# Kernel optimization log

Measured on AMD Instinct MI355X. Metric: run time of the kernel, lower is better.

Reference implementation:

```python
import jax, jax.numpy as jnp
import numpy as np

D_MODEL = 2048
K_SIZE = 4
GROUPS = 2048  # depthwise


def setup_inputs() -> dict:
    key = jax.random.key(0)
    k1, k2, k3, k4 = jax.random.split(key, 4)
    B, S, D = 4, 4096, D_MODEL
    x = jax.random.normal(k1, (B, S, D), dtype=jnp.float32)
    # nn.Linear(d_model, 3*d_model, bias=False): weight [3D, D], y = x @ W.T
    w1 = jax.random.normal(k2, (3 * D, D), dtype=jnp.float32) * (1.0 / np.sqrt(D))
    w2 = jax.random.normal(k3, (D, D), dtype=jnp.float32) * (1.0 / np.sqrt(D))
    # nn.Conv1d depthwise weight: [out_ch=D, in_ch/groups=1, k]
    conv_w = jax.random.normal(k4, (D, 1, K_SIZE), dtype=jnp.float32) * (1.0 / np.sqrt(K_SIZE))
    return {"x": x, "w1": w1, "w2": w2, "conv_w": conv_w}


def reference(x, w1, w2, conv_w):
    # x: [B, S, D]
    BCx = jnp.einsum("bsd,ed->bse", x, w1)  # [B, S, 3D]
    Bg, Cg, Xg = jnp.split(BCx, 3, axis=-1)  # each [B, S, D]
    gated = Bg * Xg
    # depthwise causal conv: torch pads k-1 both sides then slices [:seq_len]
    # == left-pad only k-1 (causal)
    y = jax.lax.conv_general_dilated(
        gated.transpose(0, 2, 1),          # [B, D, S]
        conv_w,                            # [D, 1, K]
        window_strides=(1,),
        padding=[(K_SIZE - 1, 0)],
        feature_group_count=GROUPS,
        dimension_numbers=("NCH", "OIH", "NCH"),
    )                                       # [B, D, S]
    conv_out = y.transpose(0, 2, 1)         # [B, S, D]
    out = jnp.einsum("bsd,ed->bse", Cg * conv_out, w2)  # [B, S, D]
    return out
```

## Files before the change

kernel.cpp:

```cpp
#include <hip/hip_runtime.h>
#include <stdint.h>

typedef unsigned short u16;
typedef __bf16 bf16x8 __attribute__((ext_vector_type(8)));
typedef float  f32x4  __attribute__((ext_vector_type(4)));

#define D_MODEL 2048
#define SEQ     4096
#define NROWS   16384
#define THREE_D 6144
#define K_SIZE  4
#define KC      2048
#define NT      64

__device__ __forceinline__ float b2f(u16 u) {
    union { uint32_t i; float f; } v; v.i = ((uint32_t)u) << 16; return v.f;
}
__device__ __forceinline__ u16 f2b(float f) {
    uint32_t u = __builtin_bit_cast(uint32_t, f);
    u += 0x7fff + ((u >> 16) & 1);
    return (u16)(u >> 16);
}

__global__ __launch_bounds__(256) void cast_f32_to_bf16(
    const float* __restrict__ src, u16* __restrict__ dst, int n8)
{
    int i = blockIdx.x * blockDim.x + threadIdx.x;
    if (i >= n8) return;
    const float4* s = (const float4*)src + (size_t)i * 2;
    float4 a = s[0], b = s[1];
    union { u16 u[8]; uint4 v; } o;
    o.u[0] = f2b(a.x); o.u[1] = f2b(a.y); o.u[2] = f2b(a.z); o.u[3] = f2b(a.w);
    o.u[4] = f2b(b.x); o.u[5] = f2b(b.y); o.u[6] = f2b(b.z); o.u[7] = f2b(b.w);
    *(uint4*)(dst + (size_t)i * 8) = o.v;
}

__global__ __launch_bounds__(256) void prep_cwt(
    const float* __restrict__ cw, float* __restrict__ cwt)
{
    int i = blockIdx.x * blockDim.x + threadIdx.x;
    if (i >= D_MODEL * K_SIZE) return;
    int d = i >> 2, k = i & 3;
    cwt[k * D_MODEL + d] = cw[i];
}

#define GLDS(gp, lp) __builtin_amdgcn_global_load_lds( \
    (const __attribute__((address_space(1))) void*)(gp), \
    (__attribute__((address_space(3))) void*)(lp), 16, 0, 0)

template<int BF16OUT>
__global__ __launch_bounds__(512, 2) void gemm256(
    const u16* __restrict__ A, const u16* __restrict__ B,
    void* __restrict__ Cout, int N, int n_per_xcd)
{
    __shared__ __align__(16) u16 lds[65536];

    const int tid  = threadIdx.x;
    const int lane = tid & 63;
    const int wave = tid >> 6;

    const int idx   = blockIdx.x;
    const int xcd   = idx & 7;
    const int local = idx >> 3;
    const int bm  = local / n_per_xcd;
    const int bn  = xcd * n_per_xcd + (local - bm * n_per_xcd);

    const int sfr  = tid & 15;
    const int sfq  = (tid >> 4) & 3;
    const int srow = (tid >> 6) * 16 + sfr;
    const size_t sK = (size_t)KC;
    const u16* ga = A + ((size_t)(bm * 256) + srow) * sK + sfq * 8;
    const u16* gb = B + ((size_t)(bn * 256) + srow) * sK + sfq * 8;

    u16* dst0 = lds + wave * 512;

    const int fr = lane & 15;
    const int fq = lane >> 4;
    const int wm = (wave >> 2) * 128;
    const int wn = (wave & 3) * 64;
    const int aBase = (wave >> 2) * 4096 + fq * 128 + fr * 8;
    const int bBase = 8192 + (wave & 3) * 2048 + fq * 128 + fr * 8;

    f32x4 acc[8][4] = {};

    #pragma unroll
    for (int t = 0; t < 3; t++) {
        u16* d = dst0 + t * 16384;
        const int kk = t * 32;
        GLDS(ga + kk,            d);
        GLDS(ga + 128 * sK + kk, d + 4096);
        GLDS(gb + kk,            d + 8192);
        GLDS(gb + 128 * sK + kk, d + 12288);
        __builtin_amdgcn_sched_barrier(0);
    }
    asm volatile("s_waitcnt vmcnt(8)" ::: "memory");
    __builtin_amdgcn_s_barrier();
    __builtin_amdgcn_sched_barrier(0);

    for (int t = 0; t < NT; t++) {
        const int buf = t & 3;
        if (t + 3 < NT) {
            u16* d = dst0 + ((t + 3) & 3) * 16384;
            const int kk = (t + 3) * 32;
            GLDS(ga + kk,            d);
            GLDS(ga + 128 * sK + kk, d + 4096);
            GLDS(gb + kk,            d + 8192);
            GLDS(gb + 128 * sK + kk, d + 12288);
        }
        __builtin_amdgcn_sched_barrier(0);

        bf16x8 a[8], b[4];
        const u16* la = lds + buf * 16384 + aBase;
        const u16* lb = lds + buf * 16384 + bBase;
        #pragma unroll
        for (int i = 0; i < 8; i++) a[i] = *(const bf16x8*)(la + i * 512);
        #pragma unroll
        for (int j = 0; j < 4; j++) b[j] = *(const bf16x8*)(lb + j * 512);

        __builtin_amdgcn_s_setprio(1);
        #pragma unroll
        for (int i = 0; i < 8; i++)
            #pragma unroll
            for (int j = 0; j < 4; j++)
                acc[i][j] = __builtin_amdgcn_mfma_f32_16x16x32_bf16(
                    a[i], b[j], acc[i][j], 0, 0, 0);
        __builtin_amdgcn_s_setprio(0);

        asm volatile("s_waitcnt lgkmcnt(0)" ::: "memory");
        __builtin_amdgcn_sched_barrier(0);
        if (t < NT - 3) {
            asm volatile("s_waitcnt vmcnt(8)" ::: "memory");
        } else if (t == NT - 3) {
            asm volatile("s_waitcnt vmcnt(4)" ::: "memory");
        } else if (t == NT - 2) {
            asm volatile("s_waitcnt vmcnt(0)" ::: "memory");
        }
        __builtin_amdgcn_s_barrier();
        __builtin_amdgcn_sched_barrier(0);
    }

    const int row0 = bm * 256 + wm + fq * 4;
    const int col0 = bn * 256 + wn + fr;
    if (BF16OUT) {
        u16* C = (u16*)Cout;
        #pragma unroll
        for (int i = 0; i < 8; i++)
            #pragma unroll
            for (int j = 0; j < 4; j++)
                #pragma unroll
                for (int r = 0; r < 4; r++)
                    C[(size_t)(row0 + i * 16 + r) * N + (col0 + j * 16)] = f2b(acc[i][j][r]);
    } else {
        float* C = (float*)Cout;
        #pragma unroll
        for (int i = 0; i < 8; i++)
            #pragma unroll
            for (int j = 0; j < 4; j++)
                #pragma unroll
                for (int r = 0; r < 4; r++)
                    C[(size_t)(row0 + i * 16 + r) * N + (col0 + j * 16)] = acc[i][j][r];
    }
}

__global__ __launch_bounds__(256) void gate_conv(
    const u16* __restrict__ BCx, const float* __restrict__ cwt, u16* __restrict__ z)
{
    const int n  = blockIdx.x;
    const int dg = threadIdx.x << 3;
    const int s  = n & (SEQ - 1);
    const u16* base = BCx + (size_t)n * THREE_D;

    float conv[8];
    #pragma unroll
    for (int j = 0; j < 8; j++) conv[j] = 0.f;

    #pragma unroll
    for (int r = 0; r < 4; r++) {
        const int back = 3 - r;
        if (s >= back) {
            const u16* pb = base - (size_t)back * THREE_D + dg;
            union { uint4 v; u16 u[8]; } ub, ux;
            ub.v = *(const uint4*)pb;
            ux.v = *(const uint4*)(pb + 2 * D_MODEL);
            const float* w = cwt + r * D_MODEL + dg;
            float4 w0 = *(const float4*)w;
            float4 w1 = *(const float4*)(w + 4);
            float ww[8] = { w0.x, w0.y, w0.z, w0.w, w1.x, w1.y, w1.z, w1.w };
            #pragma unroll
            for (int j = 0; j < 8; j++)
                conv[j] += b2f(ub.u[j]) * b2f(ux.u[j]) * ww[j];
        }
    }

    union { uint4 v; u16 u[8]; } uc, uo;
    uc.v = *(const uint4*)(base + D_MODEL + dg);
    #pragma unroll
    for (int j = 0; j < 8; j++)
        uo.u[j] = f2b(b2f(uc.u[j]) * conv[j]);
    *(uint4*)(z + (size_t)n * D_MODEL + dg) = uo.v;
}

extern "C" void kernel_launch(void* const* d_in, const int* in_sizes, int n_in,
                              void* d_out, int out_size, void* d_ws, size_t ws_size,
                              hipStream_t stream) {
    const float* x  = (const float*)d_in[0];
    const float* w1 = (const float*)d_in[1];
    const float* w2 = (const float*)d_in[2];
    const float* cw = (const float*)d_in[3];
    float* out = (float*)d_out;

    char* ws = (char*)d_ws;
    u16*   xb  = (u16*)(ws);
    u16*   w1b = (u16*)(ws + 67108864);
    u16*   w2b = (u16*)(ws + 92274688);
    float* cwt = (float*)(ws + 100663296);
    u16*   bcx = (u16*)(ws + 100696064);
    u16*   z   = (u16*)(ws + 302022656);

    cast_f32_to_bf16<<<dim3((4194304 + 255) / 256), 256, 0, stream>>>(x,  xb,  4194304);
    cast_f32_to_bf16<<<dim3((1572864 + 255) / 256), 256, 0, stream>>>(w1, w1b, 1572864);
    cast_f32_to_bf16<<<dim3((524288  + 255) / 256), 256, 0, stream>>>(w2, w2b, 524288);
    prep_cwt<<<dim3(32), 256, 0, stream>>>(cw, cwt);

    gemm256<1><<<dim3(1536), 512, 0, stream>>>(xb, w1b, (void*)bcx, THREE_D, 3);
    gate_conv<<<dim3(NROWS), 256, 0, stream>>>(bcx, cwt, z);
    gemm256<0><<<dim3(512), 512, 0, stream>>>(z, w2b, (void*)out, D_MODEL, 1);
}
```

Baseline: 933.3 us.

## Restructure GEMM mainloop into 64-wide K tiles with quadrant-interleaved staging

```diff
diff --git a/kernel.cpp b/kernel.cpp
--- a/kernel.cpp
+++ b/kernel.cpp
@@ -11,7 +11,7 @@
 #define THREE_D 6144
 #define K_SIZE  4
 #define KC      2048
-#define NT      64
+#define NK      32
 
 __device__ __forceinline__ float b2f(u16 u) {
     union { uint32_t i; float f; } v; v.i = ((uint32_t)u) << 16; return v.f;
@@ -57,7 +57,7 @@
 
     const int tid  = threadIdx.x;
     const int lane = tid & 63;
-    const int wave = tid >> 6;
+    const int wv   = tid >> 6;
 
     const int idx   = blockIdx.x;
     const int xcd   = idx & 7;
@@ -65,80 +65,96 @@
     const int bm  = local / n_per_xcd;
     const int bn  = xcd * n_per_xcd + (local - bm * n_per_xcd);
 
-    const int sfr  = tid & 15;
-    const int sfq  = (tid >> 4) & 3;
-    const int srow = (tid >> 6) * 16 + sfr;
+    const int sfr = tid & 15;
+    const int sfq = (tid >> 4) & 3;
+    const int gA0 = (wv & 3) + (wv >> 2) * 8;
+    const int gB0 = (wv & 1) + ((wv >> 1) & 3) * 4;
     const size_t sK = (size_t)KC;
-    const u16* ga = A + ((size_t)(bm * 256) + srow) * sK + sfq * 8;
-    const u16* gb = B + ((size_t)(bn * 256) + srow) * sK + sfq * 8;
-
-    u16* dst0 = lds + wave * 512;
+    const u16* Ab = A + ((size_t)(bm * 256) + sfr) * sK + sfq * 8;
+    const u16* Bb = B + ((size_t)(bn * 256) + sfr) * sK + sfq * 8;
+
+#define STAGE_A(g, b, k64) { \
+    GLDS(Ab + (size_t)((g) * 16) * sK + (k64),      lds + (b) * 32768 +         (g) * 512 + lane * 8); \
+    GLDS(Ab + (size_t)((g) * 16) * sK + (k64) + 32, lds + (b) * 32768 +  8192 + (g) * 512 + lane * 8); }
+#define STAGE_B(g, b, k64) { \
+    GLDS(Bb + (size_t)((g) * 16) * sK + (k64),      lds + (b) * 32768 + 16384 + (g) * 512 + lane * 8); \
+    GLDS(Bb + (size_t)((g) * 16) * sK + (k64) + 32, lds + (b) * 32768 + 24576 + (g) * 512 + lane * 8); }
 
     const int fr = lane & 15;
     const int fq = lane >> 4;
-    const int wm = (wave >> 2) * 128;
-    const int wn = (wave & 3) * 64;
-    const int aBase = (wave >> 2) * 4096 + fq * 128 + fr * 8;
-    const int bBase = 8192 + (wave & 3) * 2048 + fq * 128 + fr * 8;
+    const int aOff = (wv >> 2) * 4096 + fq * 128 + fr * 8;
+    const int bOff = 16384 + (wv & 3) * 2048 + fq * 128 + fr * 8;
 
     f32x4 acc[8][4] = {};
-
-    #pragma unroll
-    for (int t = 0; t < 3; t++) {
-        u16* d = dst0 + t * 16384;
-        const int kk = t * 32;
-        GLDS(ga + kk,            d);
-        GLDS(ga + 128 * sK + kk, d + 4096);
-        GLDS(gb + kk,            d + 8192);
-        GLDS(gb + 128 * sK + kk, d + 12288);
-        __builtin_amdgcn_sched_barrier(0);
-    }
-    asm volatile("s_waitcnt vmcnt(8)" ::: "memory");
+    bf16x8 af[4][2], bf[2][2];
+
+#define LOAD_A(buf, mh) { \
+    const u16* _p = lds + (buf) * 32768 + aOff + (mh) * 2048; \
+    _Pragma("unroll") for (int m = 0; m < 4; m++) { \
+        af[m][0] = *(const bf16x8*)(_p + m * 512); \
+        af[m][1] = *(const bf16x8*)(_p + m * 512 + 8192); } }
+#define LOAD_B(buf, nh) { \
+    const u16* _p = lds + (buf) * 32768 + bOff + (nh) * 1024; \
+    _Pragma("unroll") for (int n = 0; n < 2; n++) { \
+        bf[n][0] = *(const bf16x8*)(_p + n * 512); \
+        bf[n][1] = *(const bf16x8*)(_p + n * 512 + 8192); } }
+
+#define MFMA_Q(mh, nh) { \
+    __builtin_amdgcn_s_setprio(1); \
+    _Pragma("unroll") for (int m = 0; m < 4; m++) \
+    _Pragma("unroll") for (int n = 0; n < 2; n++) { \
+        acc[(mh)*4+m][(nh)*2+n] = __builtin_amdgcn_mfma_f32_16x16x32_bf16( \
+            af[m][0], bf[n][0], acc[(mh)*4+m][(nh)*2+n], 0, 0, 0); \
+        acc[(mh)*4+m][(nh)*2+n] = __builtin_amdgcn_mfma_f32_16x16x32_bf16( \
+            af[m][1], bf[n][1], acc[(mh)*4+m][(nh)*2+n], 0, 0, 0); } \
+    __builtin_amdgcn_s_setprio(0); }
+
+#define SYNC1 { __builtin_amdgcn_sched_barrier(0); __builtin_amdgcn_s_barrier(); \
+    asm volatile("s_waitcnt lgkmcnt(0)" ::: "memory"); __builtin_amdgcn_sched_barrier(0); }
+#define SYNC2 { __builtin_amdgcn_sched_barrier(0); __builtin_amdgcn_s_barrier(); \
+    __builtin_amdgcn_sched_barrier(0); }
+
+    STAGE_A(gA0,     0, 0);
+    STAGE_B(gB0 + 2, 0, 0);
+    STAGE_A(gA0 + 4, 0, 0);
+    STAGE_B(gB0,     0, 0);
+    STAGE_A(gA0,     1, 64);
+    STAGE_B(gB0 + 2, 1, 64);
+    STAGE_A(gA0 + 4, 1, 64);
+    __builtin_amdgcn_sched_barrier(0);
+    asm volatile("s_waitcnt vmcnt(6)" ::: "memory");
     __builtin_amdgcn_s_barrier();
     __builtin_amdgcn_sched_barrier(0);
 
-    for (int t = 0; t < NT; t++) {
-        const int buf = t & 3;
-        if (t + 3 < NT) {
-            u16* d = dst0 + ((t + 3) & 3) * 16384;
-            const int kk = (t + 3) * 32;
-            GLDS(ga + kk,            d);
-            GLDS(ga + 128 * sK + kk, d + 4096);
-            GLDS(gb + kk,            d + 8192);
-            GLDS(gb + 128 * sK + kk, d + 12288);
-        }
+    for (int kt = 0; kt < NK; kt++) {
+        const int buf = kt & 1, nbuf = buf ^ 1;
+        const int k64 = kt * 64;
+
+        LOAD_A(buf, 0); LOAD_B(buf, 0);
+        if (kt + 1 < NK) STAGE_B(gB0, nbuf, k64 + 64);
+        SYNC1; MFMA_Q(0, 0); SYNC2;
+
+        LOAD_B(buf, 1);
+        if (kt + 2 < NK) STAGE_A(gA0, buf, k64 + 128);
+        SYNC1; MFMA_Q(0, 1); SYNC2;
+
+        LOAD_A(buf, 1);
+        if (kt + 2 < NK) STAGE_B(gB0 + 2, buf, k64 + 128);
+        SYNC1; MFMA_Q(1, 1); SYNC2;
+
+        LOAD_B(buf, 0);
+        if (kt + 2 < NK) STAGE_A(gA0 + 4, buf, k64 + 128);
         __builtin_amdgcn_sched_barrier(0);
-
-        bf16x8 a[8], b[4];
-        const u16* la = lds + buf * 16384 + aBase;
-        const u16* lb = lds + buf * 16384 + bBase;
-        #pragma unroll
-        for (int i = 0; i < 8; i++) a[i] = *(const bf16x8*)(la + i * 512);
-        #pragma unroll
-        for (int j = 0; j < 4; j++) b[j] = *(const bf16x8*)(lb + j * 512);
-
-        __builtin_amdgcn_s_setprio(1);
-        #pragma unroll
-        for (int i = 0; i < 8; i++)
-            #pragma unroll
-            for (int j = 0; j < 4; j++)
-                acc[i][j] = __builtin_amdgcn_mfma_f32_16x16x32_bf16(
-                    a[i], b[j], acc[i][j], 0, 0, 0);
-        __builtin_amdgcn_s_setprio(0);
-
-        asm volatile("s_waitcnt lgkmcnt(0)" ::: "memory");
-        __builtin_amdgcn_sched_barrier(0);
-        if (t < NT - 3) {
-            asm volatile("s_waitcnt vmcnt(8)" ::: "memory");
-        } else if (t == NT - 3) {
-            asm volatile("s_waitcnt vmcnt(4)" ::: "memory");
-        } else if (t == NT - 2) {
+        if (kt < NK - 2) {
+            asm volatile("s_waitcnt vmcnt(6)" ::: "memory");
+        } else if (kt == NK - 2) {
             asm volatile("s_waitcnt vmcnt(0)" ::: "memory");
         }
-        __builtin_amdgcn_s_barrier();
-        __builtin_amdgcn_sched_barrier(0);
+        SYNC1; MFMA_Q(1, 0); SYNC2;
     }
 
+    const int wm = (wv >> 2) * 128;
+    const int wn = (wv & 3) * 64;
     const int row0 = bm * 256 + wm + fq * 4;
     const int col0 = bn * 256 + wn + fr;
     if (BF16OUT) {
@@ -160,6 +176,13 @@
                 for (int r = 0; r < 4; r++)
                     C[(size_t)(row0 + i * 16 + r) * N + (col0 + j * 16)] = acc[i][j][r];
     }
+#undef STAGE_A
+#undef STAGE_B
+#undef LOAD_A
+#undef LOAD_B
+#undef MFMA_Q
+#undef SYNC1
+#undef SYNC2
 }
 
 __global__ __launch_bounds__(256) void gate_conv(
```

Result: faster. 904.7 us (-3.1%).

## Rewrite GEMM as 4-wave 32x32x16 MFMA kernel with register double-buffering

Applied to the files above, without the earlier changes.

```diff
diff --git a/kernel.cpp b/kernel.cpp
--- a/kernel.cpp
+++ b/kernel.cpp
@@ -4,6 +4,7 @@
 typedef unsigned short u16;
 typedef __bf16 bf16x8 __attribute__((ext_vector_type(8)));
 typedef float  f32x4  __attribute__((ext_vector_type(4)));
+typedef float  f32x16 __attribute__((ext_vector_type(16)));
 
 #define D_MODEL 2048
 #define SEQ     4096
@@ -49,7 +50,7 @@
     (__attribute__((address_space(3))) void*)(lp), 16, 0, 0)
 
 template<int BF16OUT>
-__global__ __launch_bounds__(512, 2) void gemm256(
+__global__ __launch_bounds__(256, 1) void gemm_fat(
     const u16* __restrict__ A, const u16* __restrict__ B,
     void* __restrict__ Cout, int N, int n_per_xcd)
 {
@@ -57,7 +58,7 @@
 
     const int tid  = threadIdx.x;
     const int lane = tid & 63;
-    const int wave = tid >> 6;
+    const int wv   = tid >> 6;
 
     const int idx   = blockIdx.x;
     const int xcd   = idx & 7;
@@ -65,101 +66,108 @@
     const int bm  = local / n_per_xcd;
     const int bn  = xcd * n_per_xcd + (local - bm * n_per_xcd);
 
-    const int sfr  = tid & 15;
-    const int sfq  = (tid >> 4) & 3;
-    const int srow = (tid >> 6) * 16 + sfr;
     const size_t sK = (size_t)KC;
-    const u16* ga = A + ((size_t)(bm * 256) + srow) * sK + sfq * 8;
-    const u16* gb = B + ((size_t)(bn * 256) + srow) * sK + sfq * 8;
-
-    u16* dst0 = lds + wave * 512;
-
-    const int fr = lane & 15;
-    const int fq = lane >> 4;
-    const int wm = (wave >> 2) * 128;
-    const int wn = (wave & 3) * 64;
-    const int aBase = (wave >> 2) * 4096 + fq * 128 + fr * 8;
-    const int bBase = 8192 + (wave & 3) * 2048 + fq * 128 + fr * 8;
-
-    f32x4 acc[8][4] = {};
-
-    #pragma unroll
-    for (int t = 0; t < 3; t++) {
-        u16* d = dst0 + t * 16384;
-        const int kk = t * 32;
-        GLDS(ga + kk,            d);
-        GLDS(ga + 128 * sK + kk, d + 4096);
-        GLDS(gb + kk,            d + 8192);
-        GLDS(gb + 128 * sK + kk, d + 12288);
+    const int sfr = tid & 15, sq = (tid >> 4) & 3, sg = tid >> 6;
+    const u16* Ab = A + ((size_t)(bm * 256) + sg * 16 + sfr) * sK + sq * 8;
+    const u16* Bb = B + ((size_t)(bn * 256) + sg * 16 + sfr) * sK + sq * 8;
+
+    const int fr  = lane & 15;
+    const int rhi = (lane >> 4) & 1;
+    const int kh  = lane >> 5;
+    const int aoff =        ((wv >> 1) * 8 + rhi) * 512 + kh * 128 + fr * 8;
+    const int boff = 8192 + ((wv &  1) * 8 + rhi) * 512 + kh * 128 + fr * 8;
+
+    f32x16 acc[4][4] = {};
+    bf16x8 fA[8][2], fB[8][2];
+
+#define STAGE(t_) { const int _t = (t_); if (_t < NT) { \
+    const int _kk = _t * 32; \
+    u16* _d = lds + (_t & 3) * 16384 + tid * 8; \
+    GLDS(Ab + _kk,              _d); \
+    GLDS(Ab +  64 * sK + _kk,   _d + 2048); \
+    GLDS(Ab + 128 * sK + _kk,   _d + 4096); \
+    GLDS(Ab + 192 * sK + _kk,   _d + 6144); \
+    GLDS(Bb + _kk,              _d + 8192); \
+    GLDS(Bb +  64 * sK + _kk,   _d + 10240); \
+    GLDS(Bb + 128 * sK + _kk,   _d + 12288); \
+    GLDS(Bb + 192 * sK + _kk,   _d + 14336); } }
+
+#define DSREAD(t_, F) { const u16* _b = lds + ((t_) & 3) * 16384; \
+    _Pragma("unroll") for (int i = 0; i < 4; i++) { \
+        F[i][0]     = *(const bf16x8*)(_b + aoff + i * 1024); \
+        F[i][1]     = *(const bf16x8*)(_b + aoff + i * 1024 + 256); \
+        F[i + 4][0] = *(const bf16x8*)(_b + boff + i * 1024); \
+        F[i + 4][1] = *(const bf16x8*)(_b + boff + i * 1024 + 256); } }
+
+#define MM(F) { __builtin_amdgcn_s_setprio(1); \
+    _Pragma("unroll") for (int mt = 0; mt < 4; mt++) \
+    _Pragma("unroll") for (int nt = 0; nt < 4; nt++) { \
+        acc[mt][nt] = __builtin_amdgcn_mfma_f32_32x32x16_bf16( \
+            F[mt][0], F[nt + 4][0], acc[mt][nt], 0, 0, 0); \
+        acc[mt][nt] = __builtin_amdgcn_mfma_f32_32x32x16_bf16( \
+            F[mt][1], F[nt + 4][1], acc[mt][nt], 0, 0, 0); } \
+    __builtin_amdgcn_s_setprio(0); }
+
+    STAGE(0); STAGE(1); STAGE(2);
+    asm volatile("s_waitcnt vmcnt(16)" ::: "memory");
+    __builtin_amdgcn_s_barrier();
+    DSREAD(0, fA);
+
+    for (int t = 0; t < NT - 2; t += 2) {
+        asm volatile("s_waitcnt vmcnt(8)" ::: "memory");
+        __builtin_amdgcn_s_barrier();
+        STAGE(t + 3);
+        DSREAD(t + 1, fB);
+        asm volatile("s_waitcnt lgkmcnt(15)" ::: "memory");
         __builtin_amdgcn_sched_barrier(0);
+        MM(fA);
+
+        asm volatile("s_waitcnt vmcnt(8)" ::: "memory");
+        __builtin_amdgcn_s_barrier();
+        STAGE(t + 4);
+        DSREAD(t + 2, fA);
+        asm volatile("s_waitcnt lgkmcnt(15)" ::: "memory");
+        __builtin_amdgcn_sched_barrier(0);
+        MM(fB);
     }
-    asm volatile("s_waitcnt vmcnt(8)" ::: "memory");
+    asm volatile("s_waitcnt vmcnt(0)" ::: "memory");
     __builtin_amdgcn_s_barrier();
+    DSREAD(NT - 1, fB);
+    asm volatile("s_waitcnt lgkmcnt(15)" ::: "memory");
     __builtin_amdgcn_sched_barrier(0);
-
-    for (int t = 0; t < NT; t++) {
-        const int buf = t & 3;
-        if (t + 3 < NT) {
-            u16* d = dst0 + ((t + 3) & 3) * 16384;
-            const int kk = (t + 3) * 32;
-            GLDS(ga + kk,            d);
-            GLDS(ga + 128 * sK + kk, d + 4096);
-            GLDS(gb + kk,            d + 8192);
-            GLDS(gb + 128 * sK + kk, d + 12288);
-        }
-        __builtin_amdgcn_sched_barrier(0);
-
-        bf16x8 a[8], b[4];
-        const u16* la = lds + buf * 16384 + aBase;
-        const u16* lb = lds + buf * 16384 + bBase;
-        #pragma unroll
-        for (int i = 0; i < 8; i++) a[i] = *(const bf16x8*)(la + i * 512);
-        #pragma unroll
-        for (int j = 0; j < 4; j++) b[j] = *(const bf16x8*)(lb + j * 512);
-
-        __builtin_amdgcn_s_setprio(1);
-        #pragma unroll
-        for (int i = 0; i < 8; i++)
-            #pragma unroll
-            for (int j = 0; j < 4; j++)
-                acc[i][j] = __builtin_amdgcn_mfma_f32_16x16x32_bf16(
-                    a[i], b[j], acc[i][j], 0, 0, 0);
-        __builtin_amdgcn_s_setprio(0);
-
-        asm volatile("s_waitcnt lgkmcnt(0)" ::: "memory");
-        __builtin_amdgcn_sched_barrier(0);
-        if (t < NT - 3) {
-            asm volatile("s_waitcnt vmcnt(8)" ::: "memory");
-        } else if (t == NT - 3) {
-            asm volatile("s_waitcnt vmcnt(4)" ::: "memory");
-        } else if (t == NT - 2) {
-            asm volatile("s_waitcnt vmcnt(0)" ::: "memory");
-        }
-        __builtin_amdgcn_s_barrier();
-        __builtin_amdgcn_sched_barrier(0);
-    }
-
-    const int row0 = bm * 256 + wm + fq * 4;
-    const int col0 = bn * 256 + wn + fr;
+    MM(fA);
+    asm volatile("s_waitcnt lgkmcnt(0)" ::: "memory");
+    __builtin_amdgcn_sched_barrier(0);
+    MM(fB);
+
+    const int col0 = bn * 256 + (wv & 1) * 128 + (lane & 31);
+    const int rb   = bm * 256 + (wv >> 1) * 128 + kh * 4;
     if (BF16OUT) {
         u16* C = (u16*)Cout;
         #pragma unroll
-        for (int i = 0; i < 8; i++)
+        for (int mt = 0; mt < 4; mt++)
             #pragma unroll
-            for (int j = 0; j < 4; j++)
+            for (int nt = 0; nt < 4; nt++)
                 #pragma unroll
-                for (int r = 0; r < 4; r++)
-                    C[(size_t)(row0 + i * 16 + r) * N + (col0 + j * 16)] = f2b(acc[i][j][r]);
+                for (int r = 0; r < 16; r++) {
+                    const int row = rb + mt * 32 + (r & 3) + 8 * (r >> 2);
+                    C[(size_t)row * N + col0 + nt * 32] = f2b(acc[mt][nt][r]);
+                }
     } else {
         float* C = (float*)Cout;
         #pragma unroll
-        for (int i = 0; i < 8; i++)
+        for (int mt = 0; mt < 4; mt++)
             #pragma unroll
-            for (int j = 0; j < 4; j++)
+            for (int nt = 0; nt < 4; nt++)
                 #pragma unroll
-                for (int r = 0; r < 4; r++)
-                    C[(size_t)(row0 + i * 16 + r) * N + (col0 + j * 16)] = acc[i][j][r];
+                for (int r = 0; r < 16; r++) {
+                    const int row = rb + mt * 32 + (r & 3) + 8 * (r >> 2);
+                    C[(size_t)row * N + col0 + nt * 32] = acc[mt][nt][r];
+                }
     }
+#undef STAGE
+#undef DSREAD
+#undef MM
 }
 
 __global__ __launch_bounds__(256) void gate_conv(
@@ -222,7 +230,7 @@
     cast_f32_to_bf16<<<dim3((524288  + 255) / 256), 256, 0, stream>>>(w2, w2b, 524288);
     prep_cwt<<<dim3(32), 256, 0, stream>>>(cw, cwt);
 
-    gemm256<1><<<dim3(1536), 512, 0, stream>>>(xb, w1b, (void*)bcx, THREE_D, 3);
+    gemm_fat<1><<<dim3(1536), 256, 0, stream>>>(xb, w1b, (void*)bcx, THREE_D, 3);
     gate_conv<<<dim3(NROWS), 256, 0, stream>>>(bcx, cwt, z);
-    gemm256<0><<<dim3(512), 512, 0, stream>>>(z, w2b, (void*)out, D_MODEL, 1);
-}
+    gemm_fat<0><<<dim3(512), 256, 0, stream>>>(z, w2b, (void*)out, D_MODEL, 1);
+}
```

New measurement: 973.8 us. 4.3% more time.
